# Kernel tuning notes

Hardware: AMD Instinct MI355X
Metric: run time of the kernel (lower is better)

The kernel has to match this reference:

```python
import jax, jax.numpy as jnp
import numpy as np

P, E, D = 128, 32, 64          # n_proxy_sets, n_elements, d
B, SEG_LEN = 1024, 128          # number of segments, per-segment length
N = B * SEG_LEN                 # total elements


def setup_inputs() -> dict:
    key = jax.random.key(0)
    k_x, k_p = jax.random.split(key)
    x = jax.random.normal(k_x, (N, D), dtype=jnp.float32)
    proxy_sets = jax.random.normal(k_p, (P, E, D), dtype=jnp.float32)
    index = jnp.full((B,), SEG_LEN, dtype=jnp.int32)  # segment lengths, sum == N
    return {"x": x, "proxy_sets": proxy_sets, "index": index}


def reference(x, proxy_sets, index):
    # sim_mat[p,e,n] = proxy_sets[p,e,:] . x[n,:]
    sim = jnp.einsum("ped,nd->pen", proxy_sets, x)     # [P,E,N]
    t = jnp.max(sim, axis=1)                             # [P,N]  max over proxy elements
    # ragged segment sum over N driven by segment lengths `index`
    seg_ids = jnp.repeat(jnp.arange(B, dtype=jnp.int32), index,
                         total_repeat_length=N)          # [N]
    pooled = jax.ops.segment_sum(t.T, seg_ids, num_segments=B)  # [B,P]
    pooled = pooled.astype(jnp.float32)
    # F.normalize(p=2, dim=1): divide by max(||.||_2, eps)
    norm = jnp.linalg.norm(pooled, axis=1, keepdims=True)
    return pooled / jnp.maximum(norm, 1e-12)
```

## Files before the change

### kernel.cpp

```cpp
#include <hip/hip_runtime.h>
#include <stdint.h>


typedef short short8 __attribute__((ext_vector_type(8)));
typedef __bf16 bf16x8 __attribute__((ext_vector_type(8)));
typedef float floatx16 __attribute__((ext_vector_type(16)));

#define NELEM 32
#define DIM   64
#define NSEG  1024
#define LROW  68

__device__ __forceinline__ unsigned short f32_to_bf16_rne(float f) {
  union { float f; unsigned int u; } v; v.f = f;
  unsigned int r = v.u + 0x7fffu + ((v.u >> 16) & 1u);
  return (unsigned short)(r >> 16);
}

__global__ void sc_prep(const float* __restrict__ proxy,
                        const int* __restrict__ index,
                        short* __restrict__ pb2,
                        int* __restrict__ offs) {
  const int bx = blockIdx.x, t = threadIdx.x;
  if (bx == 0) {
    __shared__ int lsum[256];
    const int base = t * 4;
    const int i0 = index[base + 0], i1 = index[base + 1];
    const int i2 = index[base + 2], i3 = index[base + 3];
    const int s = i0 + i1 + i2 + i3;
    lsum[t] = s;
    __syncthreads();
    for (int off = 1; off < 256; off <<= 1) {
      int v = (t >= off) ? lsum[t - off] : 0;
      __syncthreads();
      lsum[t] += v;
      __syncthreads();
    }
    const int ex = lsum[t] - s;
    offs[base + 0] = ex;
    offs[base + 1] = ex + i0;
    offs[base + 2] = ex + i0 + i1;
    offs[base + 3] = ex + i0 + i1 + i2;
    if (t == 255) offs[NSEG] = ex + s;
  } else {
    const int w = t >> 6, lane = t & 63;
    const int task = (bx - 1) * 4 + w;
    const int p = task >> 2, kk = task & 3;
    const int l31 = lane & 31, h = lane >> 5;
    const float* src = proxy + (size_t)p * (NELEM * DIM) + l31 * DIM + kk * 16 + h * 8;
    float4 f0 = *(const float4*)(src);
    float4 f1 = *(const float4*)(src + 4);
    short8 fr;
    fr[0] = (short)f32_to_bf16_rne(f0.x);
    fr[1] = (short)f32_to_bf16_rne(f0.y);
    fr[2] = (short)f32_to_bf16_rne(f0.z);
    fr[3] = (short)f32_to_bf16_rne(f0.w);
    fr[4] = (short)f32_to_bf16_rne(f1.x);
    fr[5] = (short)f32_to_bf16_rne(f1.y);
    fr[6] = (short)f32_to_bf16_rne(f1.z);
    fr[7] = (short)f32_to_bf16_rne(f1.w);
    *(short8*)(pb2 + ((size_t)task * 64 + lane) * 8) = fr;
  }
}

__device__ __forceinline__ float max16(const floatx16& a) {
  float r0 = fmaxf(fmaxf(a[0], a[1]), a[2]);
  float r1 = fmaxf(fmaxf(a[3], a[4]), a[5]);
  float r2 = fmaxf(fmaxf(a[6], a[7]), a[8]);
  float r3 = fmaxf(fmaxf(a[9], a[10]), a[11]);
  float r4 = fmaxf(fmaxf(a[12], a[13]), a[14]);
  float r5 = fmaxf(fmaxf(r0, r1), r2);
  float r6 = fmaxf(fmaxf(r3, r4), a[15]);
  return fmaxf(r5, r6);
}

__global__ __launch_bounds__(256, 4) void sc_main(
    const float* __restrict__ x,
    const short* __restrict__ pb2,
    const int* __restrict__ offs,
    float* __restrict__ out,
    int nrows) {
  __shared__ float buf[128 * LROW];
  __shared__ float red[4];

  const int b = blockIdx.x;
  const int tid = threadIdx.x;
  const int lane = tid & 63;
  const int w = tid >> 6;
  const int wn = w & 1;
  const int wp = w >> 1;
  const int l31 = lane & 31;
  const int h = lane >> 5;

  const int start = offs[b];
  const int end = offs[b + 1];
  const int len = end - start;
  const int first = start >> 5;
  const int ntiles = (len > 0) ? (((end + 31) >> 5) - first) : 0;
  const int npass = (ntiles + 3) >> 2;

  if (ntiles == 0) {
    for (int j = tid; j < 128 * LROW; j += 256) buf[j] = 0.f;
  }

  floatx16 zc;
#pragma unroll
  for (int r = 0; r < 16; ++r) zc[r] = 0.f;

  const short* abase = pb2 + (size_t)(wp * 64) * 2048 + lane * 8;

  for (int pass = 0; pass < npass; ++pass) {
    short8 bfrag[2][4];
#pragma unroll
    for (int t4 = 0; t4 < 2; ++t4) {
      const int tile = first + pass * 4 + wn * 2 + t4;
      const int n = tile * 32 + l31;
      const bool valid = (n >= start) && (n < end) && (n < nrows);
      const float* xr = x + (size_t)(valid ? n : 0) * DIM + h * 8;
#pragma unroll
      for (int kk = 0; kk < 4; ++kk) {
        float4 f0 = make_float4(0.f, 0.f, 0.f, 0.f), f1 = f0;
        if (valid) {
          f0 = *(const float4*)(xr + kk * 16);
          f1 = *(const float4*)(xr + kk * 16 + 4);
        }
        short8 fr;
        fr[0] = (short)f32_to_bf16_rne(f0.x);
        fr[1] = (short)f32_to_bf16_rne(f0.y);
        fr[2] = (short)f32_to_bf16_rne(f0.z);
        fr[3] = (short)f32_to_bf16_rne(f0.w);
        fr[4] = (short)f32_to_bf16_rne(f1.x);
        fr[5] = (short)f32_to_bf16_rne(f1.y);
        fr[6] = (short)f32_to_bf16_rne(f1.z);
        fr[7] = (short)f32_to_bf16_rne(f1.w);
        bfrag[t4][kk] = fr;
      }
    }

    auto process = [&](int i, short8 (&cur)[4], short8 (&nxt)[4], bool pf) {
      if (pf) {
        const short* ap = abase + (size_t)(i + 1) * 2048;
#pragma unroll
        for (int kk = 0; kk < 4; ++kk)
          nxt[kk] = *(const short8*)(ap + kk * 512);
      }
      floatx16 a0, a1;
#pragma unroll
      for (int kk = 0; kk < 4; ++kk) {
        bf16x8 a = __builtin_bit_cast(bf16x8, cur[kk]);
        bf16x8 b0 = __builtin_bit_cast(bf16x8, bfrag[0][kk]);
        bf16x8 b1 = __builtin_bit_cast(bf16x8, bfrag[1][kk]);
        if (kk == 0) {
          a0 = __builtin_amdgcn_mfma_f32_32x32x16_bf16(a, b0, zc, 0, 0, 0);
          a1 = __builtin_amdgcn_mfma_f32_32x32x16_bf16(a, b1, zc, 0, 0, 0);
        } else {
          a0 = __builtin_amdgcn_mfma_f32_32x32x16_bf16(a, b0, a0, 0, 0, 0);
          a1 = __builtin_amdgcn_mfma_f32_32x32x16_bf16(a, b1, a1, 0, 0, 0);
        }
      }
      float m0 = max16(a0), m1 = max16(a1);
      m0 = fmaxf(m0, __shfl_xor(m0, 32, 64));
      m1 = fmaxf(m1, __shfl_xor(m1, 32, 64));
      const float s = m0 + m1;
      if (h == 0) {
        const int idx = (wp * 64 + i) * LROW + wn * 32 + l31;
        float prev = (pass == 0) ? 0.f : buf[idx];
        buf[idx] = prev + s;
      }
    };

    short8 afA[4], afB[4];
#pragma unroll
    for (int kk = 0; kk < 4; ++kk)
      afA[kk] = *(const short8*)(abase + kk * 512);
    for (int i = 0; i < 64; i += 2) {
      process(i, afA, afB, true);
      process(i + 1, afB, afA, i < 62);
    }
  }
  __syncthreads();

  const int p2 = tid >> 1, part = tid & 1;
  const float* bp = buf + p2 * LROW + part * 32;
  float4 v0 = *(const float4*)(bp + 0);
  float4 v1 = *(const float4*)(bp + 4);
  float4 v2 = *(const float4*)(bp + 8);
  float4 v3 = *(const float4*)(bp + 12);
  float4 v4 = *(const float4*)(bp + 16);
  float4 v5 = *(const float4*)(bp + 20);
  float4 v6 = *(const float4*)(bp + 24);
  float4 v7 = *(const float4*)(bp + 28);
  float sh = ((v0.x + v0.y) + (v0.z + v0.w)) + ((v1.x + v1.y) + (v1.z + v1.w)) +
             ((v2.x + v2.y) + (v2.z + v2.w)) + ((v3.x + v3.y) + (v3.z + v3.w)) +
             ((v4.x + v4.y) + (v4.z + v4.w)) + ((v5.x + v5.y) + (v5.z + v5.w)) +
             ((v6.x + v6.y) + (v6.z + v6.w)) + ((v7.x + v7.y) + (v7.z + v7.w));
  const float s64 = sh + __shfl_xor(sh, 1, 64);

  float sq = part ? 0.f : s64 * s64;
#pragma unroll
  for (int off = 1; off <= 32; off <<= 1) sq += __shfl_xor(sq, off, 64);
  if (lane == 0) red[w] = sq;
  __syncthreads();
  const float ss = (red[0] + red[1]) + (red[2] + red[3]);
  const float inv = 1.f / fmaxf(sqrtf(ss), 1e-12f);
  if (part == 0) out[(b << 7) + p2] = s64 * inv;
}

extern "C" void kernel_launch(void* const* d_in, const int* in_sizes, int n_in,
                              void* d_out, int out_size, void* d_ws, size_t ws_size,
                              hipStream_t stream) {
  (void)n_in; (void)out_size; (void)ws_size;
  const float* x = (const float*)d_in[0];
  const float* proxy = (const float*)d_in[1];
  const int* index = (const int*)d_in[2];
  float* out = (float*)d_out;
  const int nrows = in_sizes[0] / DIM;

  int* offs = (int*)d_ws;
  short* pb2 = (short*)((char*)d_ws + 8192);

  sc_prep<<<129, 256, 0, stream>>>(proxy, index, pb2, offs);
  sc_main<<<NSEG, 256, 0, stream>>>(x, pb2, offs, out, nrows);
}
```

Measured before the change: 138.0 us.

## Process two segments per block with each wave pair covering all proxies

Each block now handles two segments (512 blocks instead of 1024). Each pair of waves owns one segment and loops over all 128 proxy sets, rather than splitting proxies across waves. Partial sums go into shared memory through atomicAdd into a zeroed per-segment buffer, and the final normalization works per segment half. This changes the work split and the reuse of the proxy fragments, and drops the launch-bounds occupancy hint from 4 to 2. The cost is more A-fragment loads per wave, shared-memory atomics, and fewer blocks.

```diff
diff --git a/kernel.cpp b/kernel.cpp
--- a/kernel.cpp
+++ b/kernel.cpp
@@ -9,7 +9,7 @@
 #define NELEM 32
 #define DIM   64
 #define NSEG  1024
-#define LROW  68
+#define BROW  36
 
 __device__ __forceinline__ unsigned short f32_to_bf16_rne(float f) {
   union { float f; unsigned int u; } v; v.f = f;
@@ -74,48 +74,45 @@
   return fmaxf(r5, r6);
 }
 
-__global__ __launch_bounds__(256, 4) void sc_main(
+__global__ __launch_bounds__(256, 2) void sc_main(
     const float* __restrict__ x,
     const short* __restrict__ pb2,
     const int* __restrict__ offs,
     float* __restrict__ out,
     int nrows) {
-  __shared__ float buf[128 * LROW];
+  __shared__ float buf[2 * 128 * BROW];
   __shared__ float red[4];
 
   const int b = blockIdx.x;
   const int tid = threadIdx.x;
   const int lane = tid & 63;
   const int w = tid >> 6;
-  const int wn = w & 1;
-  const int wp = w >> 1;
+  const int ws = w >> 1;
+  const int wt = w & 1;
   const int l31 = lane & 31;
   const int h = lane >> 5;
 
-  const int start = offs[b];
-  const int end = offs[b + 1];
-  const int len = end - start;
-  const int first = start >> 5;
-  const int ntiles = (len > 0) ? (((end + 31) >> 5) - first) : 0;
-  const int npass = (ntiles + 3) >> 2;
-
-  if (ntiles == 0) {
-    for (int j = tid; j < 128 * LROW; j += 256) buf[j] = 0.f;
-  }
+  const int s0 = offs[2 * b + ws];
+  const int e0 = offs[2 * b + ws + 1];
+  const int len = e0 - s0;
+  const int npass = (len > 0) ? ((len + 127) >> 7) : 0;
+
+  for (int j = tid; j < 2 * 128 * BROW; j += 256) buf[j] = 0.f;
+  __syncthreads();
 
   floatx16 zc;
 #pragma unroll
   for (int r = 0; r < 16; ++r) zc[r] = 0.f;
 
-  const short* abase = pb2 + (size_t)(wp * 64) * 2048 + lane * 8;
+  const short* abase = pb2 + lane * 8;
+  float* const brow = buf + ws * 128 * BROW;
 
   for (int pass = 0; pass < npass; ++pass) {
     short8 bfrag[2][4];
 #pragma unroll
-    for (int t4 = 0; t4 < 2; ++t4) {
-      const int tile = first + pass * 4 + wn * 2 + t4;
-      const int n = tile * 32 + l31;
-      const bool valid = (n >= start) && (n < end) && (n < nrows);
+    for (int t2 = 0; t2 < 2; ++t2) {
+      const int n = s0 + pass * 128 + wt * 64 + t2 * 32 + l31;
+      const bool valid = (n < e0) && (n < nrows);
       const float* xr = x + (size_t)(valid ? n : 0) * DIM + h * 8;
 #pragma unroll
       for (int kk = 0; kk < 4; ++kk) {
@@ -133,55 +130,51 @@
         fr[5] = (short)f32_to_bf16_rne(f1.y);
         fr[6] = (short)f32_to_bf16_rne(f1.z);
         fr[7] = (short)f32_to_bf16_rne(f1.w);
-        bfrag[t4][kk] = fr;
+        bfrag[t2][kk] = fr;
       }
     }
 
-    auto process = [&](int i, short8 (&cur)[4], short8 (&nxt)[4], bool pf) {
+    auto process = [&](int p, short8 (&cur)[4], short8 (&nxt)[4], bool pf) {
       if (pf) {
-        const short* ap = abase + (size_t)(i + 1) * 2048;
+        const short* ap = abase + (size_t)(p + 1) * 2048;
 #pragma unroll
         for (int kk = 0; kk < 4; ++kk)
           nxt[kk] = *(const short8*)(ap + kk * 512);
       }
-      floatx16 a0, a1;
+      floatx16 d0, d1;
 #pragma unroll
       for (int kk = 0; kk < 4; ++kk) {
         bf16x8 a = __builtin_bit_cast(bf16x8, cur[kk]);
         bf16x8 b0 = __builtin_bit_cast(bf16x8, bfrag[0][kk]);
         bf16x8 b1 = __builtin_bit_cast(bf16x8, bfrag[1][kk]);
         if (kk == 0) {
-          a0 = __builtin_amdgcn_mfma_f32_32x32x16_bf16(a, b0, zc, 0, 0, 0);
-          a1 = __builtin_amdgcn_mfma_f32_32x32x16_bf16(a, b1, zc, 0, 0, 0);
+          d0 = __builtin_amdgcn_mfma_f32_32x32x16_bf16(a, b0, zc, 0, 0, 0);
+          d1 = __builtin_amdgcn_mfma_f32_32x32x16_bf16(a, b1, zc, 0, 0, 0);
         } else {
-          a0 = __builtin_amdgcn_mfma_f32_32x32x16_bf16(a, b0, a0, 0, 0, 0);
-          a1 = __builtin_amdgcn_mfma_f32_32x32x16_bf16(a, b1, a1, 0, 0, 0);
+          d0 = __builtin_amdgcn_mfma_f32_32x32x16_bf16(a, b0, d0, 0, 0, 0);
+          d1 = __builtin_amdgcn_mfma_f32_32x32x16_bf16(a, b1, d1, 0, 0, 0);
         }
       }
-      float m0 = max16(a0), m1 = max16(a1);
+      float m0 = max16(d0), m1 = max16(d1);
       m0 = fmaxf(m0, __shfl_xor(m0, 32, 64));
       m1 = fmaxf(m1, __shfl_xor(m1, 32, 64));
       const float s = m0 + m1;
-      if (h == 0) {
-        const int idx = (wp * 64 + i) * LROW + wn * 32 + l31;
-        float prev = (pass == 0) ? 0.f : buf[idx];
-        buf[idx] = prev + s;
-      }
+      if (h == 0)
+        atomicAdd(&brow[p * BROW + l31], s);
     };
 
-    short8 afA[4], afB[4];
+    short8 aA[4], aB[4];
 #pragma unroll
     for (int kk = 0; kk < 4; ++kk)
-      afA[kk] = *(const short8*)(abase + kk * 512);
-    for (int i = 0; i < 64; i += 2) {
-      process(i, afA, afB, true);
-      process(i + 1, afB, afA, i < 62);
+      aA[kk] = *(const short8*)(abase + kk * 512);
+    for (int p = 0; p < 128; p += 2) {
+      process(p, aA, aB, true);
+      process(p + 1, aB, aA, p < 126);
     }
   }
   __syncthreads();
 
-  const int p2 = tid >> 1, part = tid & 1;
-  const float* bp = buf + p2 * LROW + part * 32;
+  const float* bp = buf + tid * BROW;
   float4 v0 = *(const float4*)(bp + 0);
   float4 v1 = *(const float4*)(bp + 4);
   float4 v2 = *(const float4*)(bp + 8);
@@ -190,20 +183,21 @@
   float4 v5 = *(const float4*)(bp + 20);
   float4 v6 = *(const float4*)(bp + 24);
   float4 v7 = *(const float4*)(bp + 28);
-  float sh = ((v0.x + v0.y) + (v0.z + v0.w)) + ((v1.x + v1.y) + (v1.z + v1.w)) +
-             ((v2.x + v2.y) + (v2.z + v2.w)) + ((v3.x + v3.y) + (v3.z + v3.w)) +
-             ((v4.x + v4.y) + (v4.z + v4.w)) + ((v5.x + v5.y) + (v5.z + v5.w)) +
-             ((v6.x + v6.y) + (v6.z + v6.w)) + ((v7.x + v7.y) + (v7.z + v7.w));
-  const float s64 = sh + __shfl_xor(sh, 1, 64);
-
-  float sq = part ? 0.f : s64 * s64;
+  const float s32 =
+      (((v0.x + v0.y) + (v0.z + v0.w)) + ((v1.x + v1.y) + (v1.z + v1.w))) +
+      (((v2.x + v2.y) + (v2.z + v2.w)) + ((v3.x + v3.y) + (v3.z + v3.w))) +
+      (((v4.x + v4.y) + (v4.z + v4.w)) + ((v5.x + v5.y) + (v5.z + v5.w))) +
+      (((v6.x + v6.y) + (v6.z + v6.w)) + ((v7.x + v7.y) + (v7.z + v7.w)));
+
+  float sq = s32 * s32;
 #pragma unroll
   for (int off = 1; off <= 32; off <<= 1) sq += __shfl_xor(sq, off, 64);
   if (lane == 0) red[w] = sq;
   __syncthreads();
-  const float ss = (red[0] + red[1]) + (red[2] + red[3]);
+  const int ws2 = tid >> 7;
+  const float ss = red[2 * ws2] + red[2 * ws2 + 1];
   const float inv = 1.f / fmaxf(sqrtf(ss), 1e-12f);
-  if (part == 0) out[(b << 7) + p2] = s64 * inv;
+  out[(size_t)(2 * b + ws2) * 128 + (tid & 127)] = s32 * inv;
 }
 
 extern "C" void kernel_launch(void* const* d_in, const int* in_sizes, int n_in,
@@ -220,5 +214,5 @@
   short* pb2 = (short*)((char*)d_ws + 8192);
 
   sc_prep<<<129, 256, 0, stream>>>(proxy, index, pb2, offs);
-  sc_main<<<NSEG, 256, 0, stream>>>(x, pb2, offs, out, nrows);
-}
+  sc_main<<<NSEG / 2, 256, 0, stream>>>(x, pb2, offs, out, nrows);
+}
```

Measured after the change: 139.7 us. No clear change (+1.2%).
